# Kernel optimization log

Hardware: AMD Instinct MI355X
Metric: run time of the kernel (lower is better)

Reference implementation:

```python
import jax, jax.numpy as jnp
import numpy as np
from jax import lax

B, N, C = 8, 8192, 64
ODR, K, OUT = 4, 32, 128
S = N // ODR
EPS = 1e-5


def _lbr(h, W, b, g, be):
    # h: [M, K, Cin] -> linear -> BN (training-mode batch stats over (M,K) per channel) -> relu
    y = jnp.einsum('mki,oi->mko', h, W) + b
    mean = y.mean(axis=(0, 1))
    var = ((y - mean) ** 2).mean(axis=(0, 1))  # biased var, as torch BN uses for normalization
    y = (y - mean) * lax.rsqrt(var + EPS) * g + be
    return jax.nn.relu(y)


def setup_inputs() -> dict:
    key = jax.random.key(0)
    ks = jax.random.split(key, 12)
    x = jax.random.normal(ks[0], (B, N, C), dtype=jnp.float32)
    coor = jax.random.normal(ks[1], (B, N, 3), dtype=jnp.float32)
    indx = jax.random.permutation(ks[2], N)[:S]  # like torch.randperm(N)[:S]
    w1 = jax.random.normal(ks[3], (OUT, 2 * C), dtype=jnp.float32) * (2 * C) ** -0.5
    b1 = jax.random.normal(ks[4], (OUT,), dtype=jnp.float32) * 0.01
    g1 = jax.random.uniform(ks[5], (OUT,), dtype=jnp.float32, minval=0.5, maxval=1.5)
    be1 = jax.random.normal(ks[6], (OUT,), dtype=jnp.float32) * 0.01
    w2 = jax.random.normal(ks[7], (OUT, OUT), dtype=jnp.float32) * OUT ** -0.5
    b2 = jax.random.normal(ks[8], (OUT,), dtype=jnp.float32) * 0.01
    g2 = jax.random.uniform(ks[9], (OUT,), dtype=jnp.float32, minval=0.5, maxval=1.5)
    be2 = jax.random.normal(ks[10], (OUT,), dtype=jnp.float32) * 0.01
    return dict(x=x, coor=coor, indx=indx, w1=w1, b1=b1, g1=g1, be1=be1,
                w2=w2, b2=b2, g2=g2, be2=be2)


def reference(x, coor, indx, w1, b1, g1, be1, w2, b2, g2, be2):
    sampled_coor = coor[:, indx, :]  # [B,S,3]
    sampled_x = x[:, indx, :]        # [B,S,C]
    # pairwise squared distances [B,S,N]
    dist = jnp.sum((coor[:, None, :, :] - sampled_coor[:, :, None, :]) ** 2, axis=-1)
    # k smallest distances == argsort(dist)[..., :K]
    _, knn_idx = lax.top_k(-dist, K)  # [B,S,K]
    knn_x = jax.vmap(lambda xb, ib: xb[ib])(x, knn_idx)  # [B,S,K,C]
    rep_x = jnp.broadcast_to(sampled_x[:, :, None, :], (x.shape[0], S, K, x.shape[2]))
    feat = jnp.concatenate([rep_x, knn_x - rep_x], axis=-1)  # [B,S,K,2C]
    feat = feat.reshape(x.shape[0] * S, K, 2 * x.shape[2])
    h = _lbr(feat, w1, b1, g1, be1)
    h = _lbr(h, w2, b2, g2, be2)
    h = h.reshape(x.shape[0], S, K, -1)
    out = jnp.max(h, axis=2)  # [B,S,OUT]
    return out, sampled_coor
```

## Files before the change

kernel.cpp:

```cpp
#include <hip/hip_runtime.h>
#include <stdint.h>


#define N_    8192
#define GPB_  8

typedef __attribute__((ext_vector_type(8))) short bf8;
typedef __attribute__((ext_vector_type(16))) float f32x16;
typedef __attribute__((ext_vector_type(2))) float f32x2;

__device__ __forceinline__ unsigned int bf1u(float f) {
  unsigned int u = __float_as_uint(f);
  return (u + 0x7fffu + ((u >> 16) & 1u)) >> 16;
}
__device__ __forceinline__ unsigned int bfpair(float lo, float hi) {
  return bf1u(lo) | (bf1u(hi) << 16);
}

__device__ __forceinline__ f32x2 pk_add(f32x2 a, f32x2 b) {
  f32x2 d;
  asm("v_pk_add_f32 %0, %1, %2" : "=v"(d) : "v"(a), "v"(b));
  return d;
}
__device__ __forceinline__ f32x2 pk_mul(f32x2 a, f32x2 b) {
  f32x2 d;
  asm("v_pk_mul_f32 %0, %1, %2" : "=v"(d) : "v"(a), "v"(b));
  return d;
}

__global__ __launch_bounds__(256) void kprep(const float* __restrict__ w1,
                                             const float* __restrict__ w2,
                                             const float* __restrict__ coor,
                                             const int* __restrict__ indx,
                                             unsigned short* __restrict__ w1b,
                                             unsigned short* __restrict__ w2b,
                                             float* __restrict__ outc,
                                             float* __restrict__ soa) {
  int e = blockIdx.x * 256 + threadIdx.x;
  if (e < 16384) {
    w1b[e] = (unsigned short)bf1u(w1[e]);
  } else if (e < 32768) {
    int e2 = e - 16384;
    w2b[e2] = (unsigned short)bf1u(w2[e2]);
  } else if (e < 81920) {
    int e2 = e - 32768;
    int bs = e2 / 3, c = e2 - bs * 3;
    int b = bs >> 11, s = bs & 2047;
    outc[e2] = coor[(b * N_ + indx[s]) * 3 + c];
  } else {
    int p = e - 81920;
    const int b = p >> 13, i = p & 8191;
    const float* src = coor + (size_t)p * 3;
    float* dst = soa + b * 24576;
    dst[i]         = src[0];
    dst[8192 + i]  = src[1];
    dst[16384 + i] = src[2];
  }
}

__global__ __launch_bounds__(256, 8) void kknn(const float* __restrict__ soa,
                                               const int* __restrict__ indx,
                                               int* __restrict__ knn) {
  __shared__ __align__(16) float4 sdist4[4 * 256];
  __shared__ float sTw[4];
  __shared__ unsigned long long cands[192];
  __shared__ int ccnt;

  const int gid = blockIdx.x;
  const int b = gid >> 11, s = gid & 2047;
  const int tid = threadIdx.x;
  const int w = tid >> 6, lane = tid & 63;
  const float* Xb = soa + b * 24576;
  const float* Yb = Xb + 8192;
  const float* Zb = Xb + 16384;
  const int qi = indx[s];
  const float qx = Xb[qi], qy = Yb[qi], qz = Zb[qi];
  const f32x2 nqx = {-qx, -qx}, nqy = {-qy, -qy}, nqz = {-qz, -qz};

  f32x2 rd[8];
  float dmA = 3.4e38f, dmB = 3.4e38f;
#pragma unroll
  for (int it = 0; it < 8; ++it) {
    const int ofs = (it << 10) + (tid << 2);
    union { float4 f4; f32x2 h[2]; } X, Y, Z;
    X.f4 = *(const float4*)(Xb + ofs);
    Y.f4 = *(const float4*)(Yb + ofs);
    Z.f4 = *(const float4*)(Zb + ofs);
    const f32x2 dxl = pk_add(X.h[0], nqx), dyl = pk_add(Y.h[0], nqy),
                dzl = pk_add(Z.h[0], nqz);
    const f32x2 dxh = pk_add(X.h[1], nqx), dyh = pk_add(Y.h[1], nqy),
                dzh = pk_add(Z.h[1], nqz);
    const f32x2 sl =
        pk_add(pk_add(pk_mul(dxl, dxl), pk_mul(dyl, dyl)), pk_mul(dzl, dzl));
    const f32x2 sh =
        pk_add(pk_add(pk_mul(dxh, dxh), pk_mul(dyh, dyh)), pk_mul(dzh, dzh));
    dmA = fminf(fminf(sl.x, sl.y), dmA);
    dmB = fminf(fminf(sh.x, sh.y), dmB);
    if (it < 4) {
      rd[it * 2] = sl;
      rd[it * 2 + 1] = sh;
    } else {
      union { float4 f4; f32x2 h[2]; } st;
      st.h[0] = sl;
      st.h[1] = sh;
      sdist4[((it - 4) << 8) + tid] = st.f4;
    }
  }
  float dmin = fminf(dmA, dmB);
  if (tid == 0) ccnt = 0;
  if (tid < 192) cands[tid] = ~0ULL;

  float v = dmin;
#pragma unroll
  for (int k = 2; k <= 64; k <<= 1) {
#pragma unroll
    for (int j = k >> 1; j >= 1; j >>= 1) {
      const float o = __shfl_xor(v, j, 64);
      const bool dirAsc = ((lane & k) == 0);
      const bool lower = ((lane & j) == 0);
      const float lo = fminf(v, o), hi = fmaxf(v, o);
      v = (dirAsc == lower) ? lo : hi;
    }
  }
  if (lane == 7) sTw[w] = v;
  __syncthreads();
  const float T = fmaxf(fmaxf(sTw[0], sTw[1]), fmaxf(sTw[2], sTw[3]));

#pragma unroll
  for (int t = 0; t < 8; ++t) {
    const int p0 = ((t >> 1) << 10) + (tid << 2) + ((t & 1) << 1);
    const float d0 = rd[t].x, d1 = rd[t].y;
    if (d0 <= T) {
      const int pos = atomicAdd(&ccnt, 1);
      if (pos < 192)
        cands[pos] = ((unsigned long long)__float_as_uint(d0) << 32) |
                     (unsigned int)p0;
    }
    if (d1 <= T) {
      const int pos = atomicAdd(&ccnt, 1);
      if (pos < 192)
        cands[pos] = ((unsigned long long)__float_as_uint(d1) << 32) |
                     (unsigned int)(p0 + 1);
    }
  }
#pragma unroll
  for (int it = 4; it < 8; ++it) {
    const float4 d4 = sdist4[((it - 4) << 8) + tid];
    const int p0 = (it << 10) + (tid << 2);
    const float dd[4] = {d4.x, d4.y, d4.z, d4.w};
#pragma unroll
    for (int j = 0; j < 4; ++j) {
      if (dd[j] <= T) {
        const int pos = atomicAdd(&ccnt, 1);
        if (pos < 192)
          cands[pos] = ((unsigned long long)__float_as_uint(dd[j]) << 32) |
                       (unsigned int)(p0 + j);
      }
    }
  }
  __syncthreads();

  const int E = min(ccnt, 192);
  if (tid < E) {
    const unsigned long long key = cands[tid];
    int rank = 0;
    for (int j = 0; j < E; ++j) rank += (cands[j] < key) ? 1 : 0;
    if (rank < 32) knn[gid * 32 + rank] = (int)(unsigned int)key;
  }
}

template <int PHASE>
__global__ __launch_bounds__(256, 4) void kphase(
    const float* __restrict__ x, const int* __restrict__ indx,
    const int* __restrict__ knn, const float* __restrict__ b1,
    const unsigned short* __restrict__ w1b, const unsigned short* __restrict__ w2b,
    const float* __restrict__ b2, const float* __restrict__ st1,
    float* __restrict__ part, float* __restrict__ mout) {
  __shared__ __align__(16) float sx[64];
  __shared__ __align__(16) unsigned short sxb[72];
  __shared__ __align__(16) unsigned short dls[32 * 68 + 8];
  __shared__ __align__(16) unsigned short h1[PHASE == 2 ? 32 * 136 : 8];

  const int tid = threadIdx.x;
  const int w = tid >> 6;
  const int lane = tid & 63;
  const int m = lane & 31, q2 = lane >> 5;
  const int col = (w << 5) + m;
  const int r8 = tid >> 3, c8 = (tid & 7) * 8;

  const int bb = blockIdx.x & 7;
  const int jj = blockIdx.x >> 3;
  const float* xb = x + (size_t)bb * (N_ * 64);
  const int gidbase = (bb << 11) + jj * GPB_;

  bf8 bf1[8];
#pragma unroll
  for (int t = 0; t < 8; ++t)
    bf1[t] = *(const bf8*)&w1b[col * 128 + t * 16 + q2 * 8];
  bf8 bf2[8];
  float s1 = 0.f, t1 = 0.f, b2v = 0.f;
  if constexpr (PHASE == 2) {
#pragma unroll
    for (int t = 0; t < 8; ++t)
      bf2[t] = *(const bf8*)&w2b[col * 128 + t * 16 + q2 * 8];
    s1 = st1[col];
    t1 = st1[128 + col];
    b2v = b2[col];
  }
  (void)w2b; (void)b2; (void)st1; (void)mout;
  const float b1c = b1[col];

  float sum = 0.f, ssq = 0.f;

  int idxp = indx[jj * GPB_];
  float sxv = (tid < 64) ? xb[(size_t)idxp * 64 + tid] : 0.f;
  int nbr = knn[(size_t)gidbase * 32 + r8];

#pragma unroll 1
  for (int g = 0; g < GPB_; ++g) {
    const int gid = gidbase + g;
    if (tid < 64) sx[tid] = sxv;
    __syncthreads();

    {
      const float* xrow = xb + (size_t)nbr * 64 + c8;
      const float4 xa = *(const float4*)(xrow);
      const float4 xc = *(const float4*)(xrow + 4);
      const float4 sa = *(const float4*)(sx + c8);
      const float4 sc = *(const float4*)(sx + c8 + 4);
      uint2 lo, hi;
      lo.x = bfpair(xa.x - sa.x, xa.y - sa.y);
      lo.y = bfpair(xa.z - sa.z, xa.w - sa.w);
      hi.x = bfpair(xc.x - sc.x, xc.y - sc.y);
      hi.y = bfpair(xc.z - sc.z, xc.w - sc.w);
      *(uint2*)&dls[r8 * 68 + c8] = lo;
      *(uint2*)&dls[r8 * 68 + c8 + 4] = hi;
    }
    if (tid < 16) {
      const float4 sv = *(const float4*)(sx + tid * 4);
      uint2 p;
      p.x = bfpair(sv.x, sv.y);
      p.y = bfpair(sv.z, sv.w);
      *(uint2*)&sxb[tid * 4] = p;
    }

    if (g + 1 < GPB_) {
      const int s1n = jj * GPB_ + g + 1;
      const int idx1 = indx[s1n];
      sxv = (tid < 64) ? xb[(size_t)idx1 * 64 + tid] : 0.f;
      nbr = knn[(size_t)(gid + 1) * 32 + r8];
    }
    __syncthreads();

    bf8 af[8];
#pragma unroll
    for (int t = 0; t < 4; ++t) {
      union { bf8 v; uint2 u[2]; } fa;
      fa.u[0] = *(const uint2*)&sxb[t * 16 + q2 * 8];
      fa.u[1] = *(const uint2*)&sxb[t * 16 + q2 * 8 + 4];
      af[t] = fa.v;
    }
#pragma unroll
    for (int t = 0; t < 4; ++t) {
      union { bf8 v; uint2 u[2]; } fa;
      fa.u[0] = *(const uint2*)&dls[m * 68 + t * 16 + q2 * 8];
      fa.u[1] = *(const uint2*)&dls[m * 68 + t * 16 + q2 * 8 + 4];
      af[4 + t] = fa.v;
    }

    f32x16 acc;
#pragma unroll
    for (int r = 0; r < 16; ++r) acc[r] = b1c;
#pragma unroll
    for (int t = 0; t < 8; ++t)
      acc = __builtin_amdgcn_mfma_f32_32x32x16_bf16(af[t], bf1[t], acc, 0, 0, 0);

    if constexpr (PHASE == 1) {
#pragma unroll
      for (int r = 0; r < 16; ++r) {
        const float v = acc[r];
        sum += v;
        ssq = fmaf(v, v, ssq);
      }
    } else {
#pragma unroll
      for (int r = 0; r < 16; ++r) {
        const float hv = fmaxf(0.f, fmaf(acc[r], s1, t1));
        const int row = (r & 3) + ((r >> 2) << 3) + (q2 << 2);
        h1[row * 136 + col] = (unsigned short)bf1u(hv);
      }
      __syncthreads();

      f32x16 acc2;
#pragma unroll
      for (int r = 0; r < 16; ++r) acc2[r] = b2v;
#pragma unroll
      for (int t = 0; t < 8; ++t) {
        const bf8 a2 = *(const bf8*)&h1[m * 136 + t * 16 + q2 * 8];
        acc2 = __builtin_amdgcn_mfma_f32_32x32x16_bf16(a2, bf2[t], acc2, 0, 0, 0);
      }

      float mx = -1e30f;
#pragma unroll
      for (int r = 0; r < 16; ++r) {
        const float v = acc2[r];
        sum += v;
        ssq = fmaf(v, v, ssq);
        mx = fmaxf(mx, v);
      }
      mx = fmaxf(mx, __shfl_xor(mx, 32, 64));
      if (lane < 32) mout[(size_t)gid * 128 + col] = mx;
    }
  }

  sum += __shfl_xor(sum, 32, 64);
  ssq += __shfl_xor(ssq, 32, 64);
  if (lane < 32) {
    part[blockIdx.x * 256 + col] = sum;
    part[blockIdx.x * 256 + 128 + col] = ssq;
  }
}

__global__ __launch_bounds__(256) void kred1(const float* __restrict__ part,
                                             double* __restrict__ dbuf) {
  const int blk = blockIdx.x;
  const int c = threadIdx.x;
  const float* p = part + (size_t)blk * 32 * 256 + c;
  double acc = 0.0;
#pragma unroll 8
  for (int r = 0; r < 32; ++r) acc += (double)p[r * 256];
  dbuf[blk * 256 + c] = acc;
}

__global__ __launch_bounds__(256) void kred2(const double* __restrict__ dbuf,
                                             const float* __restrict__ gam,
                                             const float* __restrict__ bet,
                                             float* __restrict__ st) {
  __shared__ double sS[256];
  const int c = threadIdx.x;
  double acc = 0.0;
#pragma unroll 8
  for (int i = 0; i < 64; ++i) acc += dbuf[i * 256 + c];
  sS[c] = acc;
  __syncthreads();
  if (c < 128) {
    const double Sv = sS[c], SSv = sS[128 + c];
    const double cnt = 524288.0;
    const double mean = Sv / cnt;
    const double var = SSv / cnt - mean * mean;
    const double scale = (double)gam[c] / sqrt(var + 1e-5);
    st[c] = (float)scale;
    st[128 + c] = (float)((double)bet[c] - mean * scale);
  }
}

__global__ __launch_bounds__(256) void kout(const float* __restrict__ m,
                                            const float* __restrict__ st2,
                                            float* __restrict__ out) {
  const int e4 = blockIdx.x * 256 + threadIdx.x;
  const int o0 = (e4 & 31) * 4;
  const float4 v = ((const float4*)m)[e4];
  const float4 sc = *(const float4*)&st2[o0];
  const float4 sh = *(const float4*)&st2[128 + o0];
  float4 r;
  r.x = fmaxf(0.f, fmaf(v.x, sc.x, sh.x));
  r.y = fmaxf(0.f, fmaf(v.y, sc.y, sh.y));
  r.z = fmaxf(0.f, fmaf(v.z, sc.z, sh.z));
  r.w = fmaxf(0.f, fmaf(v.w, sc.w, sh.w));
  ((float4*)out)[e4] = r;
}

extern "C" void kernel_launch(void* const* d_in, const int* in_sizes, int n_in,
                              void* d_out, int out_size, void* d_ws, size_t ws_size,
                              hipStream_t stream) {
  (void)in_sizes; (void)n_in; (void)out_size; (void)ws_size;
  const float* x    = (const float*)d_in[0];
  const float* coor = (const float*)d_in[1];
  const int*   indx = (const int*)d_in[2];
  const float* w1   = (const float*)d_in[3];
  const float* b1   = (const float*)d_in[4];
  const float* g1   = (const float*)d_in[5];
  const float* be1  = (const float*)d_in[6];
  const float* w2   = (const float*)d_in[7];
  const float* b2   = (const float*)d_in[8];
  const float* g2   = (const float*)d_in[9];
  const float* be2  = (const float*)d_in[10];
  float* out = (float*)d_out;

  char* ws = (char*)d_ws;
  int*            knn   = (int*)(ws + 0);
  float*          mbuf  = (float*)(ws + 2097152);
  float*          part1 = (float*)(ws + 10485760);
  float*          soa   = (float*)(ws + 10485760);
  float*          part2 = (float*)(ws + 12582912);
  unsigned short* w1b   = (unsigned short*)(ws + 14680064);
  unsigned short* w2b   = (unsigned short*)(ws + 14712832);
  float*          st1   = (float*)(ws + 14745600);
  float*          st2   = (float*)(ws + 14746624);
  double*         dbuf  = (double*)(ws + 14747648);

  float* outc = out + 2097152;

  kprep<<<576, 256, 0, stream>>>(w1, w2, coor, indx, w1b, w2b, outc, soa);
  kknn<<<16384, 256, 0, stream>>>(soa, indx, knn);
  kphase<1><<<2048, 256, 0, stream>>>(x, indx, knn, b1, w1b, w2b, b2, nullptr,
                                      part1, nullptr);
  kred1<<<64, 256, 0, stream>>>(part1, dbuf);
  kred2<<<1, 256, 0, stream>>>(dbuf, g1, be1, st1);
  kphase<2><<<2048, 256, 0, stream>>>(x, indx, knn, b1, w1b, w2b, b2, st1,
                                      part2, mbuf);
  kred1<<<64, 256, 0, stream>>>(part2, dbuf);
  kred2<<<1, 256, 0, stream>>>(dbuf, g2, be2, st2);
  kout<<<2048, 256, 0, stream>>>(mbuf, st2, out);
}
```

Before: 288.7 us.

## Double-buffer LDS tiles and prefetch neighbor rows one group ahead in kphase

Removes the staging of the sampled-point row through LDS. Each thread now loads the center row it needs straight from global memory, and the neighbor-row gathers for the next group are issued one iteration ahead in registers. The dls, sxb and h1 LDS buffers are double-buffered by group parity, so one barrier per stage is enough and the earlier pre-store sync is gone; __syncthreads is replaced with an explicit lgkmcnt wait plus s_barrier. The aim is to hide gather latency and cut barrier count, at the cost of more LDS and registers, which could reduce occupancy.

New measurement: 304.3 us. +5.4%, slower.

```diff
diff --git a/kernel.cpp b/kernel.cpp
--- a/kernel.cpp
+++ b/kernel.cpp
@@ -176,10 +176,9 @@
     const unsigned short* __restrict__ w1b, const unsigned short* __restrict__ w2b,
     const float* __restrict__ b2, const float* __restrict__ st1,
     float* __restrict__ part, float* __restrict__ mout) {
-  __shared__ __align__(16) float sx[64];
-  __shared__ __align__(16) unsigned short sxb[72];
-  __shared__ __align__(16) unsigned short dls[32 * 68 + 8];
-  __shared__ __align__(16) unsigned short h1[PHASE == 2 ? 32 * 136 : 8];
+  __shared__ __align__(16) unsigned short sxb[2][80];
+  __shared__ __align__(16) unsigned short dls[2][32 * 68 + 8];
+  __shared__ __align__(16) unsigned short h1[PHASE == 2 ? 2 * 32 * 136 : 8];
 
   const int tid = threadIdx.x;
   const int w = tid >> 6;
@@ -192,6 +191,7 @@
   const int jj = blockIdx.x >> 3;
   const float* xb = x + (size_t)bb * (N_ * 64);
   const int gidbase = (bb << 11) + jj * GPB_;
+  const int sbase = jj * GPB_;
 
   bf8 bf1[8];
 #pragma unroll
@@ -212,59 +212,68 @@
 
   float sum = 0.f, ssq = 0.f;
 
-  int idxp = indx[jj * GPB_];
-  float sxv = (tid < 64) ? xb[(size_t)idxp * 64 + tid] : 0.f;
-  int nbr = knn[(size_t)gidbase * 32 + r8];
+  int idx_cur = indx[sbase];
+  const int nbr0 = knn[(size_t)gidbase * 32 + r8];
+  const float* g0row = xb + (size_t)nbr0 * 64;
+  float4 ga_c = *(const float4*)(g0row + c8);
+  float4 gc_c = *(const float4*)(g0row + c8 + 4);
+  int idx_nxt = (GPB_ > 1) ? indx[sbase + 1] : 0;
+  int nbr_nxt = (GPB_ > 1) ? knn[(size_t)(gidbase + 1) * 32 + r8] : 0;
 
 #pragma unroll 1
   for (int g = 0; g < GPB_; ++g) {
     const int gid = gidbase + g;
-    if (tid < 64) sx[tid] = sxv;
-    __syncthreads();
+    const int p = g & 1;
+
+    const float* crow = xb + (size_t)idx_cur * 64;
+    const float4 cpa = *(const float4*)(crow + c8);
+    const float4 cpc = *(const float4*)(crow + c8 + 4);
+    float4 cq;
+    if (tid < 16) cq = *(const float4*)(crow + (tid << 2));
+
+    float4 ga_n = ga_c, gc_n = gc_c;
+    if (g + 1 < GPB_) {
+      const float* grow = xb + (size_t)nbr_nxt * 64;
+      ga_n = *(const float4*)(grow + c8);
+      gc_n = *(const float4*)(grow + c8 + 4);
+    }
+    idx_cur = idx_nxt;
+    if (g + 2 < GPB_) {
+      nbr_nxt = knn[(size_t)(gid + 2) * 32 + r8];
+      idx_nxt = indx[sbase + g + 2];
+    }
 
     {
-      const float* xrow = xb + (size_t)nbr * 64 + c8;
-      const float4 xa = *(const float4*)(xrow);
-      const float4 xc = *(const float4*)(xrow + 4);
-      const float4 sa = *(const float4*)(sx + c8);
-      const float4 sc = *(const float4*)(sx + c8 + 4);
       uint2 lo, hi;
-      lo.x = bfpair(xa.x - sa.x, xa.y - sa.y);
-      lo.y = bfpair(xa.z - sa.z, xa.w - sa.w);
-      hi.x = bfpair(xc.x - sc.x, xc.y - sc.y);
-      hi.y = bfpair(xc.z - sc.z, xc.w - sc.w);
-      *(uint2*)&dls[r8 * 68 + c8] = lo;
-      *(uint2*)&dls[r8 * 68 + c8 + 4] = hi;
+      lo.x = bfpair(ga_c.x - cpa.x, ga_c.y - cpa.y);
+      lo.y = bfpair(ga_c.z - cpa.z, ga_c.w - cpa.w);
+      hi.x = bfpair(gc_c.x - cpc.x, gc_c.y - cpc.y);
+      hi.y = bfpair(gc_c.z - cpc.z, gc_c.w - cpc.w);
+      *(uint2*)&dls[p][r8 * 68 + c8] = lo;
+      *(uint2*)&dls[p][r8 * 68 + c8 + 4] = hi;
     }
     if (tid < 16) {
-      const float4 sv = *(const float4*)(sx + tid * 4);
-      uint2 p;
-      p.x = bfpair(sv.x, sv.y);
-      p.y = bfpair(sv.z, sv.w);
-      *(uint2*)&sxb[tid * 4] = p;
-    }
-
-    if (g + 1 < GPB_) {
-      const int s1n = jj * GPB_ + g + 1;
-      const int idx1 = indx[s1n];
-      sxv = (tid < 64) ? xb[(size_t)idx1 * 64 + tid] : 0.f;
-      nbr = knn[(size_t)(gid + 1) * 32 + r8];
-    }
-    __syncthreads();
+      uint2 pq;
+      pq.x = bfpair(cq.x, cq.y);
+      pq.y = bfpair(cq.z, cq.w);
+      *(uint2*)&sxb[p][tid * 4] = pq;
+    }
+    asm volatile("s_waitcnt lgkmcnt(0)" ::: "memory");
+    __builtin_amdgcn_s_barrier();
 
     bf8 af[8];
 #pragma unroll
     for (int t = 0; t < 4; ++t) {
       union { bf8 v; uint2 u[2]; } fa;
-      fa.u[0] = *(const uint2*)&sxb[t * 16 + q2 * 8];
-      fa.u[1] = *(const uint2*)&sxb[t * 16 + q2 * 8 + 4];
+      fa.u[0] = *(const uint2*)&sxb[p][t * 16 + q2 * 8];
+      fa.u[1] = *(const uint2*)&sxb[p][t * 16 + q2 * 8 + 4];
       af[t] = fa.v;
     }
 #pragma unroll
     for (int t = 0; t < 4; ++t) {
       union { bf8 v; uint2 u[2]; } fa;
-      fa.u[0] = *(const uint2*)&dls[m * 68 + t * 16 + q2 * 8];
-      fa.u[1] = *(const uint2*)&dls[m * 68 + t * 16 + q2 * 8 + 4];
+      fa.u[0] = *(const uint2*)&dls[p][m * 68 + t * 16 + q2 * 8];
+      fa.u[1] = *(const uint2*)&dls[p][m * 68 + t * 16 + q2 * 8 + 4];
       af[4 + t] = fa.v;
     }
 
@@ -283,20 +292,22 @@
         ssq = fmaf(v, v, ssq);
       }
     } else {
+      const int hp = p * (32 * 136);
 #pragma unroll
       for (int r = 0; r < 16; ++r) {
         const float hv = fmaxf(0.f, fmaf(acc[r], s1, t1));
         const int row = (r & 3) + ((r >> 2) << 3) + (q2 << 2);
-        h1[row * 136 + col] = (unsigned short)bf1u(hv);
+        h1[hp + row * 136 + col] = (unsigned short)bf1u(hv);
       }
-      __syncthreads();
+      asm volatile("s_waitcnt lgkmcnt(0)" ::: "memory");
+      __builtin_amdgcn_s_barrier();
 
       f32x16 acc2;
 #pragma unroll
       for (int r = 0; r < 16; ++r) acc2[r] = b2v;
 #pragma unroll
       for (int t = 0; t < 8; ++t) {
-        const bf8 a2 = *(const bf8*)&h1[m * 136 + t * 16 + q2 * 8];
+        const bf8 a2 = *(const bf8*)&h1[hp + m * 136 + t * 16 + q2 * 8];
         acc2 = __builtin_amdgcn_mfma_f32_32x32x16_bf16(a2, bf2[t], acc2, 0, 0, 0);
       }
 
@@ -311,6 +322,9 @@
       mx = fmaxf(mx, __shfl_xor(mx, 32, 64));
       if (lane < 32) mout[(size_t)gid * 128 + col] = mx;
     }
+
+    ga_c = ga_n;
+    gc_c = gc_n;
   }
 
   sum += __shfl_xor(sum, 32, 64);
```
